# Performance work log

Hardware: AMD Instinct MI355X
Metric: run time of the kernel (lower is better)

## Reference

```python
import math
import jax, jax.numpy as jnp
import numpy as np

B, T, C = 4, 2048, 2048
LAYER_ID, N_LAYER = 12, 24


def setup_inputs() -> dict:
    key = jax.random.key(0)
    kx, kk, kv, kr, ko = jax.random.split(key, 5)
    x = jax.random.normal(kx, (B, T, C), dtype=jnp.float32)

    # parameter init faithful to the torch __init__
    ratio_1_to_almost0 = 1.0 - LAYER_ID / N_LAYER
    ratio_0_to_1 = LAYER_ID / (N_LAYER - 1)
    h = np.arange(C, dtype=np.float64)
    zigzag = (((np.arange(C) + 1) % 3) - 1) * 0.5
    time_first = jnp.asarray(np.ones(C) * math.log(0.3) + zigzag, dtype=jnp.float32)
    base = (h / C)  # x[0,0,i] = i / n_embed
    time_mix_k = jnp.asarray((base ** ratio_1_to_almost0)[None, None, :], dtype=jnp.float32)
    time_mix_v = jnp.asarray((base ** ratio_1_to_almost0 + 0.3 * ratio_0_to_1)[None, None, :], dtype=jnp.float32)
    time_mix_r = jnp.asarray((base ** (0.5 * ratio_1_to_almost0))[None, None, :], dtype=jnp.float32)
    xx = jnp.ones((1, 1, C), dtype=jnp.float32)
    aa = jnp.ones((1, 1, C), dtype=jnp.float32)
    bb = jnp.ones((1, 1, C), dtype=jnp.float32)
    pp = jnp.full((1, 1, C), -1e30, dtype=jnp.float32)

    scale = 0.02
    w_key = jax.random.normal(kk, (C, C), dtype=jnp.float32) * scale
    w_value = jax.random.normal(kv, (C, C), dtype=jnp.float32) * scale
    w_rec = jax.random.normal(kr, (C, C), dtype=jnp.float32) * scale
    w_out = jax.random.normal(ko, (C, C), dtype=jnp.float32) * scale

    return {"x": x, "time_first": time_first, "time_mix_k": time_mix_k,
            "time_mix_v": time_mix_v, "time_mix_r": time_mix_r,
            "xx": xx, "aa": aa, "bb": bb, "pp": pp,
            "w_key": w_key, "w_value": w_value, "w_rec": w_rec, "w_out": w_out}


def reference(x, time_first, time_mix_k, time_mix_v, time_mix_r,
              xx, aa, bb, pp, w_key, w_value, w_rec, w_out):
    # token-mix against the (constant) xx state, broadcast over (B,T)
    xk = x * time_mix_k + (1.0 - time_mix_k) * xx
    xv = x * time_mix_v + (1.0 - time_mix_v) * xx
    xr = x * time_mix_r + (1.0 - time_mix_r) * xx

    # nn.Linear(bias=False): y = x @ W^T
    k = jnp.einsum('btc,oc->bto', xk, w_key)
    v = jnp.einsum('btc,oc->bto', xv, w_value)
    r = jax.nn.sigmoid(jnp.einsum('btc,oc->bto', xr, w_rec))

    t = x.shape[1]
    # F.pad(state, (0,0, 0,t-1, 0,0)) -> (1, T, C), zeros for t > 0
    aa_p = jnp.pad(aa, ((0, 0), (0, t - 1), (0, 0)))
    bb_p = jnp.pad(bb, ((0, 0), (0, t - 1), (0, 0)))
    pp_p = jnp.pad(pp, ((0, 0), (0, t - 1), (0, 0)))

    ww = time_first + k                      # (B,T,C)
    qq = jnp.maximum(pp_p, ww)
    e1 = jnp.exp(pp_p - qq)
    e2 = jnp.exp(ww - qq)
    wkv = (e1 * aa_p + e2 * v) / (e1 * bb_p + e2)

    return jnp.einsum('btc,oc->bto', r * wkv, w_out)
```

## Files before the change

### kernel.cpp

```cpp
#include <hip/hip_runtime.h>
#include <hip/hip_bf16.h>
#include <cstdint>
#include <cstddef>

using bf16    = __bf16;
using bf16x8  = __attribute__((ext_vector_type(8))) __bf16;
using floatx4 = __attribute__((ext_vector_type(4))) float;


__device__ __forceinline__ void async_cp16(const bf16* g, bf16* l) {
    __builtin_amdgcn_global_load_lds(
        (__attribute__((address_space(1))) void*)const_cast<bf16*>(g),
        (__attribute__((address_space(3))) void*)l,
        16, 0, 0);
}

__global__ __launch_bounds__(256) void prep_swz(
    const float* __restrict__ x, const float* __restrict__ tmv,
    const float* __restrict__ tmr, const float* __restrict__ xxp,
    bf16* __restrict__ xv, bf16* __restrict__ xr, int C) {
    const int t = threadIdx.x;
    const int p = t >> 6, l = t & 63;
    const int r0 = blockIdx.y << 4;
    const int c0 = blockIdx.x << 7;
    const int row = r0 + (l & 15);
    const int k = c0 + (p << 5) + ((l >> 4) << 3);

    const float4* xi = (const float4*)&x[(size_t)row * C + k];
    float4 a0 = xi[0], a1 = xi[1];
    float4 mv0 = *(const float4*)&tmv[k], mv1 = *(const float4*)&tmv[k + 4];
    float4 mr0 = *(const float4*)&tmr[k], mr1 = *(const float4*)&tmr[k + 4];
    float4 x00 = *(const float4*)&xxp[k], x01 = *(const float4*)&xxp[k + 4];

    float xa[8]  = {a0.x, a0.y, a0.z, a0.w, a1.x, a1.y, a1.z, a1.w};
    float mva[8] = {mv0.x, mv0.y, mv0.z, mv0.w, mv1.x, mv1.y, mv1.z, mv1.w};
    float mra[8] = {mr0.x, mr0.y, mr0.z, mr0.w, mr1.x, mr1.y, mr1.z, mr1.w};
    float x0a[8] = {x00.x, x00.y, x00.z, x00.w, x01.x, x01.y, x01.z, x01.w};

    bf16x8 ov, og;
#pragma unroll
    for (int u = 0; u < 8; ++u) {
        ov[u] = (bf16)(xa[u] * mva[u] + (1.0f - mva[u]) * x0a[u]);
        og[u] = (bf16)(xa[u] * mra[u] + (1.0f - mra[u]) * x0a[u]);
    }
    const size_t off = ((size_t)(r0 >> 4) * (C >> 5) + (c0 >> 5) + p) * 512 + l * 8;
    *(bf16x8*)&xv[off] = ov;
    *(bf16x8*)&xr[off] = og;
}

__global__ __launch_bounds__(256) void cvt_swz(
    const float* __restrict__ w0, const float* __restrict__ w1,
    const float* __restrict__ w2, bf16* __restrict__ o0,
    bf16* __restrict__ o1, bf16* __restrict__ o2, int C) {
    const float* w = blockIdx.z == 0 ? w0 : (blockIdx.z == 1 ? w1 : w2);
    bf16* o = blockIdx.z == 0 ? o0 : (blockIdx.z == 1 ? o1 : o2);
    const int t = threadIdx.x;
    const int p = t >> 6, l = t & 63;
    const int r0 = blockIdx.y << 4;
    const int c0 = blockIdx.x << 7;
    const int row = r0 + (l & 15);
    const int k = c0 + (p << 5) + ((l >> 4) << 3);
    const float4* wi = (const float4*)&w[(size_t)row * C + k];
    float4 a0 = wi[0], a1 = wi[1];
    float wa[8] = {a0.x, a0.y, a0.z, a0.w, a1.x, a1.y, a1.z, a1.w};
    bf16x8 ov;
#pragma unroll
    for (int u = 0; u < 8; ++u) ov[u] = (bf16)wa[u];
    const size_t off = ((size_t)(r0 >> 4) * (C >> 5) + (c0 >> 5) + p) * 512 + l * 8;
    *(bf16x8*)&o[off] = ov;
}

__global__ __launch_bounds__(256, 2) void gemm_vr(
    const bf16* __restrict__ XV, const bf16* __restrict__ XR,
    const bf16* __restrict__ WV, const bf16* __restrict__ WR,
    bf16* __restrict__ RW, int M, int N, int K) {
    __shared__ __align__(16) bf16 sXV[8192];
    __shared__ __align__(16) bf16 sXR[8192];
    __shared__ __align__(16) bf16 sWV[8192];
    __shared__ __align__(16) bf16 sWR[8192];

    const int tid  = threadIdx.x;
    const int wave = tid >> 6;
    const int lane = tid & 63;
    const int quad = lane >> 4;
    const int l16  = lane & 15;
    const int m0   = blockIdx.y * 128;
    const int n0   = blockIdx.x * 128;
    const int wm   = (wave >> 1) * 64;
    const int wn   = (wave & 1) * 64;
    const int KS   = K >> 5;

    floatx4 accv[4][4], accr[4][4];
#pragma unroll
    for (int i = 0; i < 4; ++i)
#pragma unroll
        for (int j = 0; j < 4; ++j) {
            accv[i][j] = (floatx4){0.f, 0.f, 0.f, 0.f};
            accr[i][j] = (floatx4){0.f, 0.f, 0.f, 0.f};
        }

    const size_t aoff = ((size_t)((m0 >> 4) + wave) * KS) * 512 + lane * 8;
    const size_t boff = ((size_t)((n0 >> 4) + wave) * KS) * 512 + lane * 8;
    const size_t step4 = (size_t)4 * KS * 512;
    const bf16* gXV0 = XV + aoff;
    const bf16* gXR0 = XR + aoff;
    const bf16* gWV0 = WV + boff;
    const bf16* gWR0 = WR + boff;

    const int d0 = (wave * 2) * 512;
    const int d1 = ((wave + 4) * 2) * 512;
    const int rba = (wave >> 1) * 4;
    const int rbb = (wave & 1) * 4;

    const int iters = K >> 6;
    for (int it = 0; it < iters; ++it) {
        __syncthreads();
        async_cp16(gXV0,                &sXV[d0]);
        async_cp16(gXV0 + 512,          &sXV[d0 + 512]);
        async_cp16(gXV0 + step4,        &sXV[d1]);
        async_cp16(gXV0 + step4 + 512,  &sXV[d1 + 512]);
        async_cp16(gXR0,                &sXR[d0]);
        async_cp16(gXR0 + 512,          &sXR[d0 + 512]);
        async_cp16(gXR0 + step4,        &sXR[d1]);
        async_cp16(gXR0 + step4 + 512,  &sXR[d1 + 512]);
        async_cp16(gWV0,                &sWV[d0]);
        async_cp16(gWV0 + 512,          &sWV[d0 + 512]);
        async_cp16(gWV0 + step4,        &sWV[d1]);
        async_cp16(gWV0 + step4 + 512,  &sWV[d1 + 512]);
        async_cp16(gWR0,                &sWR[d0]);
        async_cp16(gWR0 + 512,          &sWR[d0 + 512]);
        async_cp16(gWR0 + step4,        &sWR[d1]);
        async_cp16(gWR0 + step4 + 512,  &sWR[d1 + 512]);
        gXV0 += 1024; gXR0 += 1024; gWV0 += 1024; gWR0 += 1024;
        __syncthreads();

#pragma unroll
        for (int s = 0; s < 2; ++s) {
            bf16x8 av[4], bv[4];
#pragma unroll
            for (int i = 0; i < 4; ++i)
                av[i] = *(const bf16x8*)&sXV[((rba + i) * 2 + s) * 512 + (lane << 3)];
#pragma unroll
            for (int j = 0; j < 4; ++j)
                bv[j] = *(const bf16x8*)&sWV[((rbb + j) * 2 + s) * 512 + (lane << 3)];
#pragma unroll
            for (int i = 0; i < 4; ++i)
#pragma unroll
                for (int j = 0; j < 4; ++j)
                    accv[i][j] = __builtin_amdgcn_mfma_f32_16x16x32_bf16(
                        av[i], bv[j], accv[i][j], 0, 0, 0);
            bf16x8 ar[4], br[4];
#pragma unroll
            for (int i = 0; i < 4; ++i)
                ar[i] = *(const bf16x8*)&sXR[((rba + i) * 2 + s) * 512 + (lane << 3)];
#pragma unroll
            for (int j = 0; j < 4; ++j)
                br[j] = *(const bf16x8*)&sWR[((rbb + j) * 2 + s) * 512 + (lane << 3)];
#pragma unroll
            for (int i = 0; i < 4; ++i)
#pragma unroll
                for (int j = 0; j < 4; ++j)
                    accr[i][j] = __builtin_amdgcn_mfma_f32_16x16x32_bf16(
                        ar[i], br[j], accr[i][j], 0, 0, 0);
        }
    }

    const int rbase = quad * 4;
#pragma unroll
    for (int i = 0; i < 4; ++i) {
        const int rbg = ((m0 + wm) >> 4) + i;
#pragma unroll
        for (int j = 0; j < 4; ++j) {
            const int col = n0 + wn + j * 16 + l16;
            const size_t base = ((size_t)rbg * (N >> 5) + (col >> 5)) * 512 +
                                (size_t)(((col >> 3) & 3) << 4) * 8 + (col & 7);
#pragma unroll
            for (int r = 0; r < 4; ++r) {
                const float sg = 1.0f / (1.0f + __expf(-accr[i][j][r]));
                RW[base + (size_t)(rbase + r) * 8] = (bf16)(sg * accv[i][j][r]);
            }
        }
    }
}

__global__ __launch_bounds__(256) void gemm_o(
    const bf16* __restrict__ A, const bf16* __restrict__ Bw,
    float* __restrict__ Of, int M, int N, int K) {
    __shared__ __align__(16) bf16 sA[8192];
    __shared__ __align__(16) bf16 sB[8192];

    const int tid  = threadIdx.x;
    const int wave = tid >> 6;
    const int lane = tid & 63;
    const int quad = lane >> 4;
    const int l16  = lane & 15;
    const int m0   = blockIdx.y * 128;
    const int n0   = blockIdx.x * 128;
    const int wm   = (wave >> 1) * 64;
    const int wn   = (wave & 1) * 64;
    const int KS   = K >> 5;

    floatx4 acc[4][4];
#pragma unroll
    for (int i = 0; i < 4; ++i)
#pragma unroll
        for (int j = 0; j < 4; ++j) acc[i][j] = (floatx4){0.f, 0.f, 0.f, 0.f};

    const size_t step4 = (size_t)4 * KS * 512;
    const bf16* gA0 = A + ((size_t)((m0 >> 4) + wave) * KS) * 512 + lane * 8;
    const bf16* gB0 = Bw + ((size_t)((n0 >> 4) + wave) * KS) * 512 + lane * 8;
    const int d0 = (wave * 2) * 512;
    const int d1 = ((wave + 4) * 2) * 512;
    const int rba = (wave >> 1) * 4;
    const int rbb = (wave & 1) * 4;

    const int iters = K >> 6;
    for (int it = 0; it < iters; ++it) {
        __syncthreads();
        async_cp16(gA0,               &sA[d0]);
        async_cp16(gA0 + 512,         &sA[d0 + 512]);
        async_cp16(gA0 + step4,       &sA[d1]);
        async_cp16(gA0 + step4 + 512, &sA[d1 + 512]);
        async_cp16(gB0,               &sB[d0]);
        async_cp16(gB0 + 512,         &sB[d0 + 512]);
        async_cp16(gB0 + step4,       &sB[d1]);
        async_cp16(gB0 + step4 + 512, &sB[d1 + 512]);
        gA0 += 1024; gB0 += 1024;
        __syncthreads();

#pragma unroll
        for (int s = 0; s < 2; ++s) {
            bf16x8 af[4], bf[4];
#pragma unroll
            for (int i = 0; i < 4; ++i)
                af[i] = *(const bf16x8*)&sA[((rba + i) * 2 + s) * 512 + (lane << 3)];
#pragma unroll
            for (int j = 0; j < 4; ++j)
                bf[j] = *(const bf16x8*)&sB[((rbb + j) * 2 + s) * 512 + (lane << 3)];
#pragma unroll
            for (int i = 0; i < 4; ++i)
#pragma unroll
                for (int j = 0; j < 4; ++j)
                    acc[i][j] = __builtin_amdgcn_mfma_f32_16x16x32_bf16(
                        af[i], bf[j], acc[i][j], 0, 0, 0);
        }
    }

    const int rbase = quad * 4;
#pragma unroll
    for (int i = 0; i < 4; ++i) {
#pragma unroll
        for (int j = 0; j < 4; ++j) {
            const int col = n0 + wn + j * 16 + l16;
#pragma unroll
            for (int r = 0; r < 4; ++r) {
                const int row = m0 + wm + i * 16 + rbase + r;
                Of[(size_t)row * N + col] = acc[i][j][r];
            }
        }
    }
}

template <int EPI>
__global__ __launch_bounds__(256) void gemm_swz(
    const bf16* __restrict__ A, const bf16* __restrict__ Bw,
    const bf16* __restrict__ Vaux, bf16* __restrict__ Ob,
    float* __restrict__ Of, int M, int N, int K) {
    __shared__ __align__(16) bf16 sA[128 * 32];
    __shared__ __align__(16) bf16 sB[128 * 32];

    const int tid  = threadIdx.x;
    const int wave = tid >> 6;
    const int lane = tid & 63;
    const int quad = lane >> 4;
    const int l16  = lane & 15;
    const int m0   = blockIdx.y * 128;
    const int n0   = blockIdx.x * 128;
    const int wm   = (wave >> 1) * 64;
    const int wn   = (wave & 1) * 64;
    const int kslabs = K >> 5;

    floatx4 acc[4][4];
#pragma unroll
    for (int i = 0; i < 4; ++i)
#pragma unroll
        for (int j = 0; j < 4; ++j) acc[i][j] = (floatx4){0.f, 0.f, 0.f, 0.f};

    const bf16* gA0 = A + ((size_t)((m0 >> 4) + wave) * kslabs) * 512 + lane * 8;
    const bf16* gA1 = gA0 + (size_t)4 * kslabs * 512;
    const bf16* gB0 = Bw + ((size_t)((n0 >> 4) + wave) * kslabs) * 512 + lane * 8;
    const bf16* gB1 = gB0 + (size_t)4 * kslabs * 512;
    bf16* lA0 = &sA[wave * 512];
    bf16* lA1 = &sA[2048 + wave * 512];
    bf16* lB0 = &sB[wave * 512];
    bf16* lB1 = &sB[2048 + wave * 512];

    for (int it = 0; it < kslabs; ++it) {
        __syncthreads();
        async_cp16(gA0, lA0);
        async_cp16(gA1, lA1);
        async_cp16(gB0, lB0);
        async_cp16(gB1, lB1);
        gA0 += 512; gA1 += 512; gB0 += 512; gB1 += 512;
        __syncthreads();

        bf16x8 af[4], bfg[4];
#pragma unroll
        for (int i = 0; i < 4; ++i)
            af[i] = *(const bf16x8*)&sA[(((wm >> 4) + i) << 9) + (lane << 3)];
#pragma unroll
        for (int j = 0; j < 4; ++j)
            bfg[j] = *(const bf16x8*)&sB[(((wn >> 4) + j) << 9) + (lane << 3)];
#pragma unroll
        for (int i = 0; i < 4; ++i)
#pragma unroll
            for (int j = 0; j < 4; ++j)
                acc[i][j] = __builtin_amdgcn_mfma_f32_16x16x32_bf16(
                    af[i], bfg[j], acc[i][j], 0, 0, 0);
    }

    const int rbase = quad * 4;
#pragma unroll
    for (int i = 0; i < 4; ++i) {
        const int rb = ((m0 + wm) >> 4) + i;
#pragma unroll
        for (int j = 0; j < 4; ++j) {
            const int col = n0 + wn + j * 16 + l16;
            if (EPI == 2) {
#pragma unroll
                for (int r = 0; r < 4; ++r) {
                    const int row = m0 + wm + i * 16 + rbase + r;
                    Of[(size_t)row * N + col] = acc[i][j][r];
                }
            } else {
                const size_t base = ((size_t)rb * (N >> 5) + (col >> 5)) * 512 +
                                    (size_t)(((col >> 3) & 3) << 4) * 8 + (col & 7);
#pragma unroll
                for (int r = 0; r < 4; ++r) {
                    const size_t o = base + (size_t)(rbase + r) * 8;
                    const float va = acc[i][j][r];
                    if (EPI == 0) {
                        Ob[o] = (bf16)va;
                    } else {
                        const float vv = (float)Vaux[o];
                        const float sg = 1.0f / (1.0f + __expf(-va));
                        Ob[o] = (bf16)(sg * vv);
                    }
                }
            }
        }
    }
}

extern "C" void kernel_launch(void* const* d_in, const int* in_sizes, int n_in,
                              void* d_out, int out_size, void* d_ws, size_t ws_size,
                              hipStream_t stream) {
    const int C = in_sizes[1];
    const int M = in_sizes[0] / C;
    const size_t MC = (size_t)M * C;
    const size_t CC = (size_t)C * C;

    const float* x   = (const float*)d_in[0];
    const float* tmv = (const float*)d_in[3];
    const float* tmr = (const float*)d_in[4];
    const float* xxp = (const float*)d_in[5];
    const float* wv  = (const float*)d_in[10];
    const float* wr  = (const float*)d_in[11];
    const float* wo  = (const float*)d_in[12];
    float* out = (float*)d_out;

    uint8_t* ws = (uint8_t*)d_ws;
    const size_t need_full = MC * 6 + CC * 6;
    dim3 gridG(C / 128, M / 128);

    if (ws_size >= need_full) {
        bf16* xv   = (bf16*)(ws);
        bf16* xr   = (bf16*)(ws + MC * 2);
        bf16* rwkv = (bf16*)(ws + MC * 4);
        bf16* wvb  = (bf16*)(ws + MC * 6);
        bf16* wrb  = (bf16*)(ws + MC * 6 + CC * 2);
        bf16* wob  = (bf16*)(ws + MC * 6 + CC * 4);

        prep_swz<<<dim3(C / 128, M / 16), 256, 0, stream>>>(x, tmv, tmr, xxp, xv, xr, C);
        cvt_swz<<<dim3(C / 128, C / 16, 3), 256, 0, stream>>>(wv, wr, wo, wvb, wrb, wob, C);
        gemm_vr<<<gridG, 256, 0, stream>>>(xv, xr, wvb, wrb, rwkv, M, C, C);
        gemm_o<<<gridG, 256, 0, stream>>>(rwkv, wob, out, M, C, C);
    } else {
        bf16* xv   = (bf16*)(ws);
        bf16* xr   = (bf16*)(ws + MC * 2);
        bf16* vbuf = (bf16*)d_out;
        bf16* wvb  = (bf16*)(ws + MC * 4);
        bf16* wrb  = (bf16*)(ws + MC * 4 + CC * 2);
        bf16* wob  = (bf16*)(ws + MC * 4 + CC * 4);
        bf16* rwkv = xv;

        prep_swz<<<dim3(C / 128, M / 16), 256, 0, stream>>>(x, tmv, tmr, xxp, xv, xr, C);
        cvt_swz<<<dim3(C / 128, C / 16, 3), 256, 0, stream>>>(wv, wr, wo, wvb, wrb, wob, C);
        gemm_swz<0><<<gridG, 256, 0, stream>>>(xv, wvb, nullptr, vbuf, nullptr, M, C, C);
        gemm_swz<1><<<gridG, 256, 0, stream>>>(xr, wrb, vbuf, rwkv, nullptr, M, C, C);
        gemm_swz<2><<<gridG, 256, 0, stream>>>(rwkv, wob, nullptr, nullptr, out, M, C, C);
    }
}
```

Baseline: 401.8 us.

## Merge prep/convert kernels, remap GEMM blocks per XCD, widen output GEMM tile

```diff
diff --git a/kernel.cpp b/kernel.cpp
--- a/kernel.cpp
+++ b/kernel.cpp
@@ -15,59 +15,63 @@
         16, 0, 0);
 }
 
-__global__ __launch_bounds__(256) void prep_swz(
+__global__ __launch_bounds__(256) void prep_cvt(
     const float* __restrict__ x, const float* __restrict__ tmv,
     const float* __restrict__ tmr, const float* __restrict__ xxp,
-    bf16* __restrict__ xv, bf16* __restrict__ xr, int C) {
+    const float* __restrict__ w0, const float* __restrict__ w1,
+    const float* __restrict__ w2, bf16* __restrict__ xv, bf16* __restrict__ xr,
+    bf16* __restrict__ o0, bf16* __restrict__ o1, bf16* __restrict__ o2,
+    int C, int prepRows) {
     const int t = threadIdx.x;
     const int p = t >> 6, l = t & 63;
-    const int r0 = blockIdx.y << 4;
     const int c0 = blockIdx.x << 7;
-    const int row = r0 + (l & 15);
     const int k = c0 + (p << 5) + ((l >> 4) << 3);
-
-    const float4* xi = (const float4*)&x[(size_t)row * C + k];
-    float4 a0 = xi[0], a1 = xi[1];
-    float4 mv0 = *(const float4*)&tmv[k], mv1 = *(const float4*)&tmv[k + 4];
-    float4 mr0 = *(const float4*)&tmr[k], mr1 = *(const float4*)&tmr[k + 4];
-    float4 x00 = *(const float4*)&xxp[k], x01 = *(const float4*)&xxp[k + 4];
-
-    float xa[8]  = {a0.x, a0.y, a0.z, a0.w, a1.x, a1.y, a1.z, a1.w};
-    float mva[8] = {mv0.x, mv0.y, mv0.z, mv0.w, mv1.x, mv1.y, mv1.z, mv1.w};
-    float mra[8] = {mr0.x, mr0.y, mr0.z, mr0.w, mr1.x, mr1.y, mr1.z, mr1.w};
-    float x0a[8] = {x00.x, x00.y, x00.z, x00.w, x01.x, x01.y, x01.z, x01.w};
-
-    bf16x8 ov, og;
-#pragma unroll
-    for (int u = 0; u < 8; ++u) {
-        ov[u] = (bf16)(xa[u] * mva[u] + (1.0f - mva[u]) * x0a[u]);
-        og[u] = (bf16)(xa[u] * mra[u] + (1.0f - mra[u]) * x0a[u]);
-    }
-    const size_t off = ((size_t)(r0 >> 4) * (C >> 5) + (c0 >> 5) + p) * 512 + l * 8;
-    *(bf16x8*)&xv[off] = ov;
-    *(bf16x8*)&xr[off] = og;
-}
-
-__global__ __launch_bounds__(256) void cvt_swz(
-    const float* __restrict__ w0, const float* __restrict__ w1,
-    const float* __restrict__ w2, bf16* __restrict__ o0,
-    bf16* __restrict__ o1, bf16* __restrict__ o2, int C) {
-    const float* w = blockIdx.z == 0 ? w0 : (blockIdx.z == 1 ? w1 : w2);
-    bf16* o = blockIdx.z == 0 ? o0 : (blockIdx.z == 1 ? o1 : o2);
-    const int t = threadIdx.x;
-    const int p = t >> 6, l = t & 63;
-    const int r0 = blockIdx.y << 4;
-    const int c0 = blockIdx.x << 7;
-    const int row = r0 + (l & 15);
-    const int k = c0 + (p << 5) + ((l >> 4) << 3);
-    const float4* wi = (const float4*)&w[(size_t)row * C + k];
-    float4 a0 = wi[0], a1 = wi[1];
-    float wa[8] = {a0.x, a0.y, a0.z, a0.w, a1.x, a1.y, a1.z, a1.w};
-    bf16x8 ov;
-#pragma unroll
-    for (int u = 0; u < 8; ++u) ov[u] = (bf16)wa[u];
-    const size_t off = ((size_t)(r0 >> 4) * (C >> 5) + (c0 >> 5) + p) * 512 + l * 8;
-    *(bf16x8*)&o[off] = ov;
+    const int yb = blockIdx.y;
+    const int C4 = C >> 4;
+
+    if (yb < prepRows) {
+        const int r0 = yb << 4;
+        const int row = r0 + (l & 15);
+        const float4* xi = (const float4*)&x[(size_t)row * C + k];
+        float4 a0 = xi[0], a1 = xi[1];
+        float4 mv0 = *(const float4*)&tmv[k], mv1 = *(const float4*)&tmv[k + 4];
+        float4 mr0 = *(const float4*)&tmr[k], mr1 = *(const float4*)&tmr[k + 4];
+        float4 x00 = *(const float4*)&xxp[k], x01 = *(const float4*)&xxp[k + 4];
+        float xa[8]  = {a0.x, a0.y, a0.z, a0.w, a1.x, a1.y, a1.z, a1.w};
+        float mva[8] = {mv0.x, mv0.y, mv0.z, mv0.w, mv1.x, mv1.y, mv1.z, mv1.w};
+        float mra[8] = {mr0.x, mr0.y, mr0.z, mr0.w, mr1.x, mr1.y, mr1.z, mr1.w};
+        float x0a[8] = {x00.x, x00.y, x00.z, x00.w, x01.x, x01.y, x01.z, x01.w};
+        bf16x8 ov, og;
+#pragma unroll
+        for (int u = 0; u < 8; ++u) {
+            ov[u] = (bf16)(xa[u] * mva[u] + (1.0f - mva[u]) * x0a[u]);
+            og[u] = (bf16)(xa[u] * mra[u] + (1.0f - mra[u]) * x0a[u]);
+        }
+        const size_t off = ((size_t)(r0 >> 4) * (C >> 5) + (c0 >> 5) + p) * 512 + l * 8;
+        *(bf16x8*)&xv[off] = ov;
+        *(bf16x8*)&xr[off] = og;
+    } else {
+        int z = yb - prepRows;
+        const float* wsrc;
+        bf16* wdst;
+        if (z < C4) {
+            wsrc = w0; wdst = o0;
+        } else if (z < 2 * C4) {
+            wsrc = w1; wdst = o1; z -= C4;
+        } else {
+            wsrc = w2; wdst = o2; z -= 2 * C4;
+        }
+        const int r0 = z << 4;
+        const int row = r0 + (l & 15);
+        const float4* wi = (const float4*)&wsrc[(size_t)row * C + k];
+        float4 a0 = wi[0], a1 = wi[1];
+        float wa[8] = {a0.x, a0.y, a0.z, a0.w, a1.x, a1.y, a1.z, a1.w};
+        bf16x8 ov;
+#pragma unroll
+        for (int u = 0; u < 8; ++u) ov[u] = (bf16)wa[u];
+        const size_t off = ((size_t)(r0 >> 4) * (C >> 5) + (c0 >> 5) + p) * 512 + l * 8;
+        *(bf16x8*)&wdst[off] = ov;
+    }
 }
 
 __global__ __launch_bounds__(256, 2) void gemm_vr(
@@ -79,13 +83,19 @@
     __shared__ __align__(16) bf16 sWV[8192];
     __shared__ __align__(16) bf16 sWR[8192];
 
+    const int bid = blockIdx.x;
+    const int xcd = bid & 7;
+    const int tt  = bid >> 3;
+    const int mt  = xcd * 8 + (tt & 7);
+    const int nt  = tt >> 3;
+
     const int tid  = threadIdx.x;
     const int wave = tid >> 6;
     const int lane = tid & 63;
     const int quad = lane >> 4;
     const int l16  = lane & 15;
-    const int m0   = blockIdx.y * 128;
-    const int n0   = blockIdx.x * 128;
+    const int m0   = mt * 128;
+    const int n0   = nt * 128;
     const int wm   = (wave >> 1) * 64;
     const int wn   = (wave & 1) * 64;
     const int KS   = K >> 5;
@@ -183,66 +193,74 @@
     }
 }
 
-__global__ __launch_bounds__(256) void gemm_o(
+__global__ __launch_bounds__(256, 2) void gemm_o(
     const bf16* __restrict__ A, const bf16* __restrict__ Bw,
     float* __restrict__ Of, int M, int N, int K) {
     __shared__ __align__(16) bf16 sA[8192];
-    __shared__ __align__(16) bf16 sB[8192];
+    __shared__ __align__(16) bf16 sB[16384];
+
+    const int bid = blockIdx.x;
+    const int xcd = bid & 7;
+    const int tt  = bid >> 3;
+    const int mt  = xcd * 8 + (tt & 7);
+    const int nt  = tt >> 3;
 
     const int tid  = threadIdx.x;
     const int wave = tid >> 6;
     const int lane = tid & 63;
     const int quad = lane >> 4;
     const int l16  = lane & 15;
-    const int m0   = blockIdx.y * 128;
-    const int n0   = blockIdx.x * 128;
+    const int m0   = mt * 128;
+    const int n0   = nt * 256;
     const int wm   = (wave >> 1) * 64;
-    const int wn   = (wave & 1) * 64;
+    const int wnb  = (wave & 1) * 128;
     const int KS   = K >> 5;
 
-    floatx4 acc[4][4];
+    floatx4 acc[4][8];
 #pragma unroll
     for (int i = 0; i < 4; ++i)
 #pragma unroll
-        for (int j = 0; j < 4; ++j) acc[i][j] = (floatx4){0.f, 0.f, 0.f, 0.f};
+        for (int j = 0; j < 8; ++j) acc[i][j] = (floatx4){0.f, 0.f, 0.f, 0.f};
 
     const size_t step4 = (size_t)4 * KS * 512;
     const bf16* gA0 = A + ((size_t)((m0 >> 4) + wave) * KS) * 512 + lane * 8;
     const bf16* gB0 = Bw + ((size_t)((n0 >> 4) + wave) * KS) * 512 + lane * 8;
-    const int d0 = (wave * 2) * 512;
-    const int d1 = ((wave + 4) * 2) * 512;
+    const int dA0 = (wave * 2) * 512;
+    const int dA1 = ((wave + 4) * 2) * 512;
     const int rba = (wave >> 1) * 4;
-    const int rbb = (wave & 1) * 4;
+    const int rbb = (wave & 1) * 8;
 
     const int iters = K >> 6;
     for (int it = 0; it < iters; ++it) {
         __syncthreads();
-        async_cp16(gA0,               &sA[d0]);
-        async_cp16(gA0 + 512,         &sA[d0 + 512]);
-        async_cp16(gA0 + step4,       &sA[d1]);
-        async_cp16(gA0 + step4 + 512, &sA[d1 + 512]);
-        async_cp16(gB0,               &sB[d0]);
-        async_cp16(gB0 + 512,         &sB[d0 + 512]);
-        async_cp16(gB0 + step4,       &sB[d1]);
-        async_cp16(gB0 + step4 + 512, &sB[d1 + 512]);
+        async_cp16(gA0,               &sA[dA0]);
+        async_cp16(gA0 + 512,         &sA[dA0 + 512]);
+        async_cp16(gA0 + step4,       &sA[dA1]);
+        async_cp16(gA0 + step4 + 512, &sA[dA1 + 512]);
+#pragma unroll
+        for (int u = 0; u < 4; ++u) {
+            const int dB = ((wave + 4 * u) * 2) * 512;
+            async_cp16(gB0 + u * step4,       &sB[dB]);
+            async_cp16(gB0 + u * step4 + 512, &sB[dB + 512]);
+        }
         gA0 += 1024; gB0 += 1024;
         __syncthreads();
 
 #pragma unroll
         for (int s = 0; s < 2; ++s) {
-            bf16x8 af[4], bf[4];
+            bf16x8 af[4], bfg[8];
 #pragma unroll
             for (int i = 0; i < 4; ++i)
                 af[i] = *(const bf16x8*)&sA[((rba + i) * 2 + s) * 512 + (lane << 3)];
 #pragma unroll
-            for (int j = 0; j < 4; ++j)
-                bf[j] = *(const bf16x8*)&sB[((rbb + j) * 2 + s) * 512 + (lane << 3)];
-#pragma unroll
-            for (int i = 0; i < 4; ++i)
-#pragma unroll
-                for (int j = 0; j < 4; ++j)
+            for (int j = 0; j < 8; ++j)
+                bfg[j] = *(const bf16x8*)&sB[((rbb + j) * 2 + s) * 512 + (lane << 3)];
+#pragma unroll
+            for (int i = 0; i < 4; ++i)
+#pragma unroll
+                for (int j = 0; j < 8; ++j)
                     acc[i][j] = __builtin_amdgcn_mfma_f32_16x16x32_bf16(
-                        af[i], bf[j], acc[i][j], 0, 0, 0);
+                        af[i], bfg[j], acc[i][j], 0, 0, 0);
         }
     }
 
@@ -250,8 +268,8 @@
 #pragma unroll
     for (int i = 0; i < 4; ++i) {
 #pragma unroll
-        for (int j = 0; j < 4; ++j) {
-            const int col = n0 + wn + j * 16 + l16;
+        for (int j = 0; j < 8; ++j) {
+            const int col = n0 + wnb + j * 16 + l16;
 #pragma unroll
             for (int r = 0; r < 4; ++r) {
                 const int row = m0 + wm + i * 16 + rbase + r;
@@ -371,7 +389,8 @@
 
     uint8_t* ws = (uint8_t*)d_ws;
     const size_t need_full = MC * 6 + CC * 6;
-    dim3 gridG(C / 128, M / 128);
+    const int prepRows = M / 16;
+    dim3 gridP(C / 128, M / 16 + 3 * (C / 16));
 
     if (ws_size >= need_full) {
         bf16* xv   = (bf16*)(ws);
@@ -381,10 +400,11 @@
         bf16* wrb  = (bf16*)(ws + MC * 6 + CC * 2);
         bf16* wob  = (bf16*)(ws + MC * 6 + CC * 4);
 
-        prep_swz<<<dim3(C / 128, M / 16), 256, 0, stream>>>(x, tmv, tmr, xxp, xv, xr, C);
-        cvt_swz<<<dim3(C / 128, C / 16, 3), 256, 0, stream>>>(wv, wr, wo, wvb, wrb, wob, C);
-        gemm_vr<<<gridG, 256, 0, stream>>>(xv, xr, wvb, wrb, rwkv, M, C, C);
-        gemm_o<<<gridG, 256, 0, stream>>>(rwkv, wob, out, M, C, C);
+        prep_cvt<<<gridP, 256, 0, stream>>>(x, tmv, tmr, xxp, wv, wr, wo,
+                                            xv, xr, wvb, wrb, wob, C, prepRows);
+        gemm_vr<<<(M / 128) * (C / 128), 256, 0, stream>>>(xv, xr, wvb, wrb, rwkv,
+                                                           M, C, C);
+        gemm_o<<<(M / 128) * (C / 256), 256, 0, stream>>>(rwkv, wob, out, M, C, C);
     } else {
         bf16* xv   = (bf16*)(ws);
         bf16* xr   = (bf16*)(ws + MC * 2);
@@ -394,8 +414,9 @@
         bf16* wob  = (bf16*)(ws + MC * 4 + CC * 4);
         bf16* rwkv = xv;
 
-        prep_swz<<<dim3(C / 128, M / 16), 256, 0, stream>>>(x, tmv, tmr, xxp, xv, xr, C);
-        cvt_swz<<<dim3(C / 128, C / 16, 3), 256, 0, stream>>>(wv, wr, wo, wvb, wrb, wob, C);
+        dim3 gridG(C / 128, M / 128);
+        prep_cvt<<<gridP, 256, 0, stream>>>(x, tmv, tmr, xxp, wv, wr, wo,
+                                            xv, xr, wvb, wrb, wob, C, prepRows);
         gemm_swz<0><<<gridG, 256, 0, stream>>>(xv, wvb, nullptr, vbuf, nullptr, M, C, C);
         gemm_swz<1><<<gridG, 256, 0, stream>>>(xr, wrb, vbuf, rwkv, nullptr, M, C, C);
         gemm_swz<2><<<gridG, 256, 0, stream>>>(rwkv, wob, nullptr, nullptr, out, M, C, C);
```

After: 372.0 us. 1.08x faster.
